# Kernel tuning notes

Hardware: AMD Instinct MI355X
Metric: run time of the kernel (lower is better)

## Reference

```python
import jax, jax.numpy as jnp
import numpy as np

V = 20000
D = 128
N_PAIRS = 65536
LOG_EPS = 1e-8


def setup_inputs() -> dict:
    key = jax.random.key(0)
    k_emb, k_i, k_j = jax.random.split(key, 3)
    # original: tf.random.uniform([V, D], 0.1, -0.1) -> uniform in (-0.1, 0.1)
    embedding = jax.random.uniform(k_emb, (V, D), dtype=jnp.float32) * 0.2 - 0.1
    i_vec = jax.random.randint(k_i, (N_PAIRS,), 0, V, dtype=jnp.int64)
    j_vec = jax.random.randint(k_j, (N_PAIRS,), 0, V, dtype=jnp.int64)
    return {"embedding": embedding, "i_vec": i_vec, "j_vec": j_vec}


def reference(embedding, i_vec, j_vec):
    # norms[i] = exp( sum_j e_i . e_j )  -- full V x V Gram matrix row-reduced
    gram = jnp.matmul(embedding, embedding.T)        # [V, V]
    norms = jnp.exp(jnp.sum(gram, axis=1))           # [V]
    # denoms[p] = exp( e_{i_p} . e_{j_p} )
    denoms = jnp.exp(jnp.sum(embedding[i_vec] * embedding[j_vec], axis=1))  # [N]
    emb_cost = -jnp.log(denoms / norms[i_vec] + LOG_EPS)
    return jnp.mean(emb_cost)
```

## Files before the change

kernel.cpp:

```cpp
#include <hip/hip_runtime.h>
#include <math.h>

#define DIM     128
#define V_ROWS  20000
#define NPAIRS  65536
#define NFLOAT4 (V_ROWS * DIM / 4)

constexpr int K1_BLOCKS  = 256;
constexpr int K1_THREADS = 256;
constexpr int K1_STRIDE  = K1_BLOCKS * K1_THREADS;
constexpr int K3_BLOCKS  = 1024;
constexpr int K3_THREADS = 256;


__global__ __launch_bounds__(K1_THREADS) void k1_colsum(
        const float4* __restrict__ emb4,
        float* __restrict__ partial) {
    const int tid = blockIdx.x * K1_THREADS + threadIdx.x;
    float4 a = make_float4(0.f, 0.f, 0.f, 0.f);
    #pragma unroll
    for (int k = 0; k < 9; ++k) {
        const float4 v = emb4[tid + k * K1_STRIDE];
        a.x += v.x; a.y += v.y; a.z += v.z; a.w += v.w;
    }
    if (tid + 9 * K1_STRIDE < NFLOAT4) {
        const float4 v = emb4[tid + 9 * K1_STRIDE];
        a.x += v.x; a.y += v.y; a.z += v.z; a.w += v.w;
    }
    a.x += __shfl_xor(a.x, 32);
    a.y += __shfl_xor(a.y, 32);
    a.z += __shfl_xor(a.z, 32);
    a.w += __shfl_xor(a.w, 32);

    __shared__ float sm[4][DIM];
    const int wid  = threadIdx.x >> 6;
    const int lane = threadIdx.x & 63;
    const int col  = (threadIdx.x * 4) & 127;
    if (lane < 32) {
        sm[wid][col + 0] = a.x;
        sm[wid][col + 1] = a.y;
        sm[wid][col + 2] = a.z;
        sm[wid][col + 3] = a.w;
    }
    __syncthreads();
    if (threadIdx.x < DIM) {
        partial[blockIdx.x * DIM + threadIdx.x] =
            sm[0][threadIdx.x] + sm[1][threadIdx.x] +
            sm[2][threadIdx.x] + sm[3][threadIdx.x];
    }
}

__global__ __launch_bounds__(1024) void k2_fold(
        const float* __restrict__ partial,
        float* __restrict__ S) {
    const int t   = threadIdx.x;
    const int col = t & 127;
    const int g   = t >> 7;
    float s = 0.f;
    #pragma unroll
    for (int k = 0; k < 32; ++k) {
        s += partial[(g + k * 8) * DIM + col];
    }
    __shared__ float sm[8][DIM];
    sm[g][col] = s;
    __syncthreads();
    if (t < DIM) {
        float tot = 0.f;
        #pragma unroll
        for (int g2 = 0; g2 < 8; ++g2) tot += sm[g2][t];
        S[t] = tot;
    }
}

__global__ __launch_bounds__(K3_THREADS) void k3_pairs(
        const float4* __restrict__ emb4,
        const int* __restrict__ iv,
        const int* __restrict__ jv,
        const float* __restrict__ S,
        float* __restrict__ blockpart) {
    const int lane = threadIdx.x & 63;
    const int wid  = threadIdx.x >> 6;
    const int c    = lane & 15;
    const int grp  = lane >> 4;
    const int gw   = blockIdx.x * 4 + wid;
    const int base = gw * 16;

    const float4* S4 = reinterpret_cast<const float4*>(S);
    const float4 s0 = S4[c * 2], s1 = S4[c * 2 + 1];

    int idxval = 0;
    if (lane < 16)      idxval = iv[base + lane];
    else if (lane < 32) idxval = jv[base + lane - 16];

    float4 A0[4], A1[4], B0[4], B1[4];
    #pragma unroll
    for (int it = 0; it < 4; ++it) {
        const int q = it * 4 + grp;
        const int i = __shfl(idxval, q);
        const int j = __shfl(idxval, 16 + q);
        const float4* ei = emb4 + (size_t)i * 32;
        const float4* ej = emb4 + (size_t)j * 32;
        A0[it] = ei[c * 2]; A1[it] = ei[c * 2 + 1];
        B0[it] = ej[c * 2]; B1[it] = ej[c * 2 + 1];
    }

    float acc = 0.f;
    #pragma unroll
    for (int it = 0; it < 4; ++it) {
        float d = A0[it].x * B0[it].x + A0[it].y * B0[it].y
                + A0[it].z * B0[it].z + A0[it].w * B0[it].w
                + A1[it].x * B1[it].x + A1[it].y * B1[it].y
                + A1[it].z * B1[it].z + A1[it].w * B1[it].w;
        float n = A0[it].x * s0.x + A0[it].y * s0.y
                + A0[it].z * s0.z + A0[it].w * s0.w
                + A1[it].x * s1.x + A1[it].y * s1.y
                + A1[it].z * s1.z + A1[it].w * s1.w;
        #pragma unroll
        for (int off = 8; off > 0; off >>= 1) {
            d += __shfl_xor(d, off);
            n += __shfl_xor(n, off);
        }
        const float cost = -logf(expf(d - n) + 1e-8f);
        if (c == 0) acc += cost;
    }

    acc += __shfl_xor(acc, 16);
    acc += __shfl_xor(acc, 32);

    __shared__ float ls[4];
    if (lane == 0) ls[wid] = acc;
    __syncthreads();
    if (threadIdx.x == 0)
        blockpart[blockIdx.x] = ls[0] + ls[1] + ls[2] + ls[3];
}

__global__ __launch_bounds__(1024) void k4_final(
        const float* __restrict__ blockpart,
        float* __restrict__ out) {
    const int t = threadIdx.x;
    float s = blockpart[t];
    #pragma unroll
    for (int off = 32; off > 0; off >>= 1) s += __shfl_xor(s, off);
    __shared__ float ls[16];
    if ((t & 63) == 0) ls[t >> 6] = s;
    __syncthreads();
    if (t == 0) {
        float tot = 0.f;
        #pragma unroll
        for (int w = 0; w < 16; ++w) tot += ls[w];
        out[0] = tot / (float)NPAIRS;
    }
}

extern "C" void kernel_launch(void* const* d_in, const int* in_sizes, int n_in,
                              void* d_out, int out_size, void* d_ws, size_t ws_size,
                              hipStream_t stream) {
    const float* emb = (const float*)d_in[0];
    const int*   iv  = (const int*)d_in[1];
    const int*   jv  = (const int*)d_in[2];
    float* out = (float*)d_out;

    float* partial   = (float*)d_ws;
    float* S         = partial + K1_BLOCKS * DIM;
    float* blockpart = S + DIM;

    hipLaunchKernelGGL(k1_colsum, dim3(K1_BLOCKS), dim3(K1_THREADS), 0, stream,
                       (const float4*)emb, partial);
    hipLaunchKernelGGL(k2_fold, dim3(1), dim3(1024), 0, stream,
                       partial, S);
    hipLaunchKernelGGL(k3_pairs, dim3(K3_BLOCKS), dim3(K3_THREADS), 0, stream,
                       (const float4*)emb, iv, jv, S, blockpart);
    hipLaunchKernelGGL(k4_final, dim3(1), dim3(1024), 0, stream,
                       blockpart, out);
}
```

Measured before the change: 23.48 us.

## Fuse four kernels into one cooperative kernel with grid-wide syncs

Replaces the colsum, fold, pair-loss and final-reduce launches with a single cooperative kernel of 256 blocks that uses grid.sync between phases. Each block redundantly folds the column partials into shared memory instead of a dedicated single-block kernel, and each wave now processes 64 pairs across four outer iterations. The aim is to remove launch gaps and tiny serial kernels, at the cost of grid-barrier overhead and fewer waves in flight for the gather phase.

```diff
diff --git a/kernel.cpp b/kernel.cpp
--- a/kernel.cpp
+++ b/kernel.cpp
@@ -1,175 +1,164 @@
 #include <hip/hip_runtime.h>
+#include <hip/hip_cooperative_groups.h>
 #include <math.h>
+
+namespace cg = cooperative_groups;
 
 #define DIM     128
 #define V_ROWS  20000
 #define NPAIRS  65536
 #define NFLOAT4 (V_ROWS * DIM / 4)
 
-constexpr int K1_BLOCKS  = 256;
-constexpr int K1_THREADS = 256;
-constexpr int K1_STRIDE  = K1_BLOCKS * K1_THREADS;
-constexpr int K3_BLOCKS  = 1024;
-constexpr int K3_THREADS = 256;
+constexpr int BLOCKS  = 256;
+constexpr int THREADS = 256;
+constexpr int NTHREADS = BLOCKS * THREADS;
+constexpr int TAIL = NFLOAT4 - 9 * NTHREADS;
 
 
-__global__ __launch_bounds__(K1_THREADS) void k1_colsum(
-        const float4* __restrict__ emb4,
-        float* __restrict__ partial) {
-    const int tid = blockIdx.x * K1_THREADS + threadIdx.x;
-    float4 a = make_float4(0.f, 0.f, 0.f, 0.f);
-    #pragma unroll
-    for (int k = 0; k < 9; ++k) {
-        const float4 v = emb4[tid + k * K1_STRIDE];
-        a.x += v.x; a.y += v.y; a.z += v.z; a.w += v.w;
-    }
-    if (tid + 9 * K1_STRIDE < NFLOAT4) {
-        const float4 v = emb4[tid + 9 * K1_STRIDE];
-        a.x += v.x; a.y += v.y; a.z += v.z; a.w += v.w;
-    }
-    a.x += __shfl_xor(a.x, 32);
-    a.y += __shfl_xor(a.y, 32);
-    a.z += __shfl_xor(a.z, 32);
-    a.w += __shfl_xor(a.w, 32);
-
-    __shared__ float sm[4][DIM];
-    const int wid  = threadIdx.x >> 6;
-    const int lane = threadIdx.x & 63;
-    const int col  = (threadIdx.x * 4) & 127;
-    if (lane < 32) {
-        sm[wid][col + 0] = a.x;
-        sm[wid][col + 1] = a.y;
-        sm[wid][col + 2] = a.z;
-        sm[wid][col + 3] = a.w;
-    }
-    __syncthreads();
-    if (threadIdx.x < DIM) {
-        partial[blockIdx.x * DIM + threadIdx.x] =
-            sm[0][threadIdx.x] + sm[1][threadIdx.x] +
-            sm[2][threadIdx.x] + sm[3][threadIdx.x];
-    }
-}
-
-__global__ __launch_bounds__(1024) void k2_fold(
-        const float* __restrict__ partial,
-        float* __restrict__ S) {
-    const int t   = threadIdx.x;
-    const int col = t & 127;
-    const int g   = t >> 7;
-    float s = 0.f;
-    #pragma unroll
-    for (int k = 0; k < 32; ++k) {
-        s += partial[(g + k * 8) * DIM + col];
-    }
-    __shared__ float sm[8][DIM];
-    sm[g][col] = s;
-    __syncthreads();
-    if (t < DIM) {
-        float tot = 0.f;
-        #pragma unroll
-        for (int g2 = 0; g2 < 8; ++g2) tot += sm[g2][t];
-        S[t] = tot;
-    }
-}
-
-__global__ __launch_bounds__(K3_THREADS) void k3_pairs(
+__global__ __launch_bounds__(THREADS) void fused(
         const float4* __restrict__ emb4,
         const int* __restrict__ iv,
         const int* __restrict__ jv,
-        const float* __restrict__ S,
-        float* __restrict__ blockpart) {
+        float* __restrict__ partial,
+        float* __restrict__ blockpart,
+        float* __restrict__ out) {
+    const cg::grid_group grid = cg::this_grid();
     const int lane = threadIdx.x & 63;
     const int wid  = threadIdx.x >> 6;
-    const int c    = lane & 15;
-    const int grp  = lane >> 4;
-    const int gw   = blockIdx.x * 4 + wid;
-    const int base = gw * 16;
 
-    const float4* S4 = reinterpret_cast<const float4*>(S);
-    const float4 s0 = S4[c * 2], s1 = S4[c * 2 + 1];
+    __shared__ float sm[4][DIM];
+    __shared__ float S_lds[DIM];
+    __shared__ float ls[4];
 
-    int idxval = 0;
-    if (lane < 16)      idxval = iv[base + lane];
-    else if (lane < 32) idxval = jv[base + lane - 16];
+    {
+        const int tid = blockIdx.x * THREADS + threadIdx.x;
+        float4 a = make_float4(0.f, 0.f, 0.f, 0.f);
+        #pragma unroll
+        for (int k = 0; k < 9; ++k) {
+            const float4 v = emb4[tid + k * NTHREADS];
+            a.x += v.x; a.y += v.y; a.z += v.z; a.w += v.w;
+        }
+        if (tid < TAIL) {
+            const float4 v = emb4[tid + 9 * NTHREADS];
+            a.x += v.x; a.y += v.y; a.z += v.z; a.w += v.w;
+        }
+        a.x += __shfl_xor(a.x, 32);
+        a.y += __shfl_xor(a.y, 32);
+        a.z += __shfl_xor(a.z, 32);
+        a.w += __shfl_xor(a.w, 32);
 
-    float4 A0[4], A1[4], B0[4], B1[4];
-    #pragma unroll
-    for (int it = 0; it < 4; ++it) {
-        const int q = it * 4 + grp;
-        const int i = __shfl(idxval, q);
-        const int j = __shfl(idxval, 16 + q);
-        const float4* ei = emb4 + (size_t)i * 32;
-        const float4* ej = emb4 + (size_t)j * 32;
-        A0[it] = ei[c * 2]; A1[it] = ei[c * 2 + 1];
-        B0[it] = ej[c * 2]; B1[it] = ej[c * 2 + 1];
+        const int col = (threadIdx.x * 4) & 127;
+        if (lane < 32) {
+            sm[wid][col + 0] = a.x;
+            sm[wid][col + 1] = a.y;
+            sm[wid][col + 2] = a.z;
+            sm[wid][col + 3] = a.w;
+        }
+        __syncthreads();
+        if (threadIdx.x < DIM) {
+            partial[blockIdx.x * DIM + threadIdx.x] =
+                sm[0][threadIdx.x] + sm[1][threadIdx.x] +
+                sm[2][threadIdx.x] + sm[3][threadIdx.x];
+        }
     }
 
-    float acc = 0.f;
-    #pragma unroll
-    for (int it = 0; it < 4; ++it) {
-        float d = A0[it].x * B0[it].x + A0[it].y * B0[it].y
-                + A0[it].z * B0[it].z + A0[it].w * B0[it].w
-                + A1[it].x * B1[it].x + A1[it].y * B1[it].y
-                + A1[it].z * B1[it].z + A1[it].w * B1[it].w;
-        float n = A0[it].x * s0.x + A0[it].y * s0.y
-                + A0[it].z * s0.z + A0[it].w * s0.w
-                + A1[it].x * s1.x + A1[it].y * s1.y
-                + A1[it].z * s1.z + A1[it].w * s1.w;
-        #pragma unroll
-        for (int off = 8; off > 0; off >>= 1) {
-            d += __shfl_xor(d, off);
-            n += __shfl_xor(n, off);
+    grid.sync();
+
+    {
+        const int col = threadIdx.x & 127;
+        const int g   = threadIdx.x >> 7;
+        float s = 0.f;
+        #pragma unroll 8
+        for (int k = 0; k < BLOCKS / 2; ++k) {
+            s += partial[(g + 2 * k) * DIM + col];
         }
-        const float cost = -logf(expf(d - n) + 1e-8f);
-        if (c == 0) acc += cost;
+        __syncthreads();
+        sm[g][col] = s;
+        __syncthreads();
+        if (threadIdx.x < DIM) S_lds[threadIdx.x] = sm[0][threadIdx.x] + sm[1][threadIdx.x];
+        __syncthreads();
     }
 
-    acc += __shfl_xor(acc, 16);
-    acc += __shfl_xor(acc, 32);
+    {
+        const int c   = lane & 15;
+        const int grp = lane >> 4;
+        const int gw  = blockIdx.x * 4 + wid;
+        const int base = gw * 64;
 
-    __shared__ float ls[4];
-    if (lane == 0) ls[wid] = acc;
-    __syncthreads();
-    if (threadIdx.x == 0)
-        blockpart[blockIdx.x] = ls[0] + ls[1] + ls[2] + ls[3];
-}
+        const float4* S4 = reinterpret_cast<const float4*>(S_lds);
+        const float4 s0 = S4[c * 2], s1 = S4[c * 2 + 1];
 
-__global__ __launch_bounds__(1024) void k4_final(
-        const float* __restrict__ blockpart,
-        float* __restrict__ out) {
-    const int t = threadIdx.x;
-    float s = blockpart[t];
-    #pragma unroll
-    for (int off = 32; off > 0; off >>= 1) s += __shfl_xor(s, off);
-    __shared__ float ls[16];
-    if ((t & 63) == 0) ls[t >> 6] = s;
-    __syncthreads();
-    if (t == 0) {
-        float tot = 0.f;
+        const int i64 = iv[base + lane];
+        const int j64 = jv[base + lane];
+
+        float acc = 0.f;
+        for (int ot = 0; ot < 4; ++ot) {
+            float4 A0[4], A1[4], B0[4], B1[4];
+            #pragma unroll
+            for (int it = 0; it < 4; ++it) {
+                const int q = ot * 16 + it * 4 + grp;
+                const int i = __shfl(i64, q);
+                const int j = __shfl(j64, q);
+                const float4* ei = emb4 + (size_t)i * 32;
+                const float4* ej = emb4 + (size_t)j * 32;
+                A0[it] = ei[c * 2]; A1[it] = ei[c * 2 + 1];
+                B0[it] = ej[c * 2]; B1[it] = ej[c * 2 + 1];
+            }
+            #pragma unroll
+            for (int it = 0; it < 4; ++it) {
+                float d = A0[it].x * B0[it].x + A0[it].y * B0[it].y
+                        + A0[it].z * B0[it].z + A0[it].w * B0[it].w
+                        + A1[it].x * B1[it].x + A1[it].y * B1[it].y
+                        + A1[it].z * B1[it].z + A1[it].w * B1[it].w;
+                float n = A0[it].x * s0.x + A0[it].y * s0.y
+                        + A0[it].z * s0.z + A0[it].w * s0.w
+                        + A1[it].x * s1.x + A1[it].y * s1.y
+                        + A1[it].z * s1.z + A1[it].w * s1.w;
+                #pragma unroll
+                for (int off = 8; off > 0; off >>= 1) {
+                    d += __shfl_xor(d, off);
+                    n += __shfl_xor(n, off);
+                }
+                const float cost = -logf(expf(d - n) + 1e-8f);
+                if (c == 0) acc += cost;
+            }
+        }
+        acc += __shfl_xor(acc, 16);
+        acc += __shfl_xor(acc, 32);
+
+        __syncthreads();
+        if (lane == 0) ls[wid] = acc;
+        __syncthreads();
+        if (threadIdx.x == 0)
+            blockpart[blockIdx.x] = ls[0] + ls[1] + ls[2] + ls[3];
+    }
+
+    grid.sync();
+
+    if (blockIdx.x == 0) {
+        float s = blockpart[threadIdx.x];
         #pragma unroll
-        for (int w = 0; w < 16; ++w) tot += ls[w];
-        out[0] = tot / (float)NPAIRS;
+        for (int off = 32; off > 0; off >>= 1) s += __shfl_xor(s, off);
+        if (lane == 0) ls[wid] = s;
+        __syncthreads();
+        if (threadIdx.x == 0)
+            out[0] = (ls[0] + ls[1] + ls[2] + ls[3]) / (float)NPAIRS;
     }
 }
 
 extern "C" void kernel_launch(void* const* d_in, const int* in_sizes, int n_in,
                               void* d_out, int out_size, void* d_ws, size_t ws_size,
                               hipStream_t stream) {
-    const float* emb = (const float*)d_in[0];
-    const int*   iv  = (const int*)d_in[1];
-    const int*   jv  = (const int*)d_in[2];
+    const float4* emb4 = (const float4*)d_in[0];
+    const int*    iv   = (const int*)d_in[1];
+    const int*    jv   = (const int*)d_in[2];
     float* out = (float*)d_out;
 
     float* partial   = (float*)d_ws;
-    float* S         = partial + K1_BLOCKS * DIM;
-    float* blockpart = S + DIM;
+    float* blockpart = partial + BLOCKS * DIM;
 
-    hipLaunchKernelGGL(k1_colsum, dim3(K1_BLOCKS), dim3(K1_THREADS), 0, stream,
-                       (const float4*)emb, partial);
-    hipLaunchKernelGGL(k2_fold, dim3(1), dim3(1024), 0, stream,
-                       partial, S);
-    hipLaunchKernelGGL(k3_pairs, dim3(K3_BLOCKS), dim3(K3_THREADS), 0, stream,
-                       (const float4*)emb, iv, jv, S, blockpart);
-    hipLaunchKernelGGL(k4_final, dim3(1), dim3(1024), 0, stream,
-                       blockpart, out);
+    void* args[] = { (void*)&emb4, (void*)&iv, (void*)&jv,
+                     (void*)&partial, (void*)&blockpart, (void*)&out };
+    hipLaunchCooperativeKernel((const void*)fused, dim3(BLOCKS), dim3(THREADS),
+                               args, 0, stream);
 }
```

Result: slower. 77.92 us (+231.9%).

## Fuse column-sum fold into pairs kernel and double pairs per warp

Applied to the files above, without the earlier changes.

Removes the single-block fold kernel by having every block of the pairs kernel redundantly reduce the 256 partial column sums into shared memory. Each warp now processes 32 pairs in two batches, halving the grid to 512 blocks, and the final reduction shrinks to 256 threads. This saves one kernel launch and its serial dependency, but each block re-reads the 128 KB of partials, which adds L2 traffic and startup latency per block.

```diff
diff --git a/kernel.cpp b/kernel.cpp
--- a/kernel.cpp
+++ b/kernel.cpp
@@ -9,8 +9,10 @@
 constexpr int K1_BLOCKS  = 256;
 constexpr int K1_THREADS = 256;
 constexpr int K1_STRIDE  = K1_BLOCKS * K1_THREADS;
-constexpr int K3_BLOCKS  = 1024;
-constexpr int K3_THREADS = 256;
+constexpr int K1_TAIL    = NFLOAT4 - 9 * K1_STRIDE;
+
+constexpr int K2_BLOCKS  = 512;
+constexpr int K2_THREADS = 256;
 
 
 __global__ __launch_bounds__(K1_THREADS) void k1_colsum(
@@ -23,7 +25,7 @@
         const float4 v = emb4[tid + k * K1_STRIDE];
         a.x += v.x; a.y += v.y; a.z += v.z; a.w += v.w;
     }
-    if (tid + 9 * K1_STRIDE < NFLOAT4) {
+    if (tid < K1_TAIL) {
         const float4 v = emb4[tid + 9 * K1_STRIDE];
         a.x += v.x; a.y += v.y; a.z += v.z; a.w += v.w;
     }
@@ -50,126 +52,118 @@
     }
 }
 
-__global__ __launch_bounds__(1024) void k2_fold(
-        const float* __restrict__ partial,
-        float* __restrict__ S) {
-    const int t   = threadIdx.x;
-    const int col = t & 127;
-    const int g   = t >> 7;
-    float s = 0.f;
-    #pragma unroll
-    for (int k = 0; k < 32; ++k) {
-        s += partial[(g + k * 8) * DIM + col];
-    }
-    __shared__ float sm[8][DIM];
-    sm[g][col] = s;
-    __syncthreads();
-    if (t < DIM) {
-        float tot = 0.f;
-        #pragma unroll
-        for (int g2 = 0; g2 < 8; ++g2) tot += sm[g2][t];
-        S[t] = tot;
-    }
-}
-
-__global__ __launch_bounds__(K3_THREADS) void k3_pairs(
+__global__ __launch_bounds__(K2_THREADS) void k2_pairs(
         const float4* __restrict__ emb4,
         const int* __restrict__ iv,
         const int* __restrict__ jv,
-        const float* __restrict__ S,
+        const float* __restrict__ partial,
         float* __restrict__ blockpart) {
     const int lane = threadIdx.x & 63;
     const int wid  = threadIdx.x >> 6;
+
+    __shared__ float sm[2][DIM];
+    __shared__ float S_lds[DIM];
+    __shared__ float ls[4];
+
+    {
+        const int col = threadIdx.x & 127;
+        const int g   = threadIdx.x >> 7;
+        float s0 = 0.f, s1 = 0.f, s2 = 0.f, s3 = 0.f;
+        #pragma unroll 8
+        for (int k = 0; k < 32; ++k) {
+            s0 += partial[(g + 8 * k + 0) * DIM + col];
+            s1 += partial[(g + 8 * k + 2) * DIM + col];
+            s2 += partial[(g + 8 * k + 4) * DIM + col];
+            s3 += partial[(g + 8 * k + 6) * DIM + col];
+        }
+        sm[g][col] = (s0 + s1) + (s2 + s3);
+        __syncthreads();
+        if (threadIdx.x < DIM)
+            S_lds[threadIdx.x] = sm[0][threadIdx.x] + sm[1][threadIdx.x];
+        __syncthreads();
+    }
+
     const int c    = lane & 15;
     const int grp  = lane >> 4;
     const int gw   = blockIdx.x * 4 + wid;
-    const int base = gw * 16;
+    const int base = gw * 32;
 
-    const float4* S4 = reinterpret_cast<const float4*>(S);
+    const float4* S4 = reinterpret_cast<const float4*>(S_lds);
     const float4 s0 = S4[c * 2], s1 = S4[c * 2 + 1];
 
-    int idxval = 0;
-    if (lane < 16)      idxval = iv[base + lane];
-    else if (lane < 32) idxval = jv[base + lane - 16];
-
-    float4 A0[4], A1[4], B0[4], B1[4];
-    #pragma unroll
-    for (int it = 0; it < 4; ++it) {
-        const int q = it * 4 + grp;
-        const int i = __shfl(idxval, q);
-        const int j = __shfl(idxval, 16 + q);
-        const float4* ei = emb4 + (size_t)i * 32;
-        const float4* ej = emb4 + (size_t)j * 32;
-        A0[it] = ei[c * 2]; A1[it] = ei[c * 2 + 1];
-        B0[it] = ej[c * 2]; B1[it] = ej[c * 2 + 1];
-    }
+    const int idxval = (lane < 32) ? iv[base + lane] : jv[base + lane - 32];
 
     float acc = 0.f;
     #pragma unroll
-    for (int it = 0; it < 4; ++it) {
-        float d = A0[it].x * B0[it].x + A0[it].y * B0[it].y
-                + A0[it].z * B0[it].z + A0[it].w * B0[it].w
-                + A1[it].x * B1[it].x + A1[it].y * B1[it].y
-                + A1[it].z * B1[it].z + A1[it].w * B1[it].w;
-        float n = A0[it].x * s0.x + A0[it].y * s0.y
-                + A0[it].z * s0.z + A0[it].w * s0.w
-                + A1[it].x * s1.x + A1[it].y * s1.y
-                + A1[it].z * s1.z + A1[it].w * s1.w;
+    for (int ot = 0; ot < 2; ++ot) {
+        float4 A0[4], A1[4], B0[4], B1[4];
         #pragma unroll
-        for (int off = 8; off > 0; off >>= 1) {
-            d += __shfl_xor(d, off);
-            n += __shfl_xor(n, off);
+        for (int it = 0; it < 4; ++it) {
+            const int q = ot * 16 + it * 4 + grp;
+            const int i = __shfl(idxval, q);
+            const int j = __shfl(idxval, 32 + q);
+            const float4* ei = emb4 + (size_t)i * 32;
+            const float4* ej = emb4 + (size_t)j * 32;
+            A0[it] = ei[c * 2]; A1[it] = ei[c * 2 + 1];
+            B0[it] = ej[c * 2]; B1[it] = ej[c * 2 + 1];
         }
-        const float cost = -logf(expf(d - n) + 1e-8f);
-        if (c == 0) acc += cost;
+        #pragma unroll
+        for (int it = 0; it < 4; ++it) {
+            float d = A0[it].x * B0[it].x + A0[it].y * B0[it].y
+                    + A0[it].z * B0[it].z + A0[it].w * B0[it].w
+                    + A1[it].x * B1[it].x + A1[it].y * B1[it].y
+                    + A1[it].z * B1[it].z + A1[it].w * B1[it].w;
+            float n = A0[it].x * s0.x + A0[it].y * s0.y
+                    + A0[it].z * s0.z + A0[it].w * s0.w
+                    + A1[it].x * s1.x + A1[it].y * s1.y
+                    + A1[it].z * s1.z + A1[it].w * s1.w;
+            #pragma unroll
+            for (int off = 8; off > 0; off >>= 1) {
+                d += __shfl_xor(d, off);
+                n += __shfl_xor(n, off);
+            }
+            const float cost = -logf(expf(d - n) + 1e-8f);
+            if (c == 0) acc += cost;
+        }
     }
-
     acc += __shfl_xor(acc, 16);
     acc += __shfl_xor(acc, 32);
 
-    __shared__ float ls[4];
     if (lane == 0) ls[wid] = acc;
     __syncthreads();
     if (threadIdx.x == 0)
         blockpart[blockIdx.x] = ls[0] + ls[1] + ls[2] + ls[3];
 }
 
-__global__ __launch_bounds__(1024) void k4_final(
+__global__ __launch_bounds__(256) void k3_final(
         const float* __restrict__ blockpart,
         float* __restrict__ out) {
     const int t = threadIdx.x;
-    float s = blockpart[t];
+    float s = blockpart[t] + blockpart[t + 256];
     #pragma unroll
     for (int off = 32; off > 0; off >>= 1) s += __shfl_xor(s, off);
-    __shared__ float ls[16];
+    __shared__ float ls[4];
     if ((t & 63) == 0) ls[t >> 6] = s;
     __syncthreads();
-    if (t == 0) {
-        float tot = 0.f;
-        #pragma unroll
-        for (int w = 0; w < 16; ++w) tot += ls[w];
-        out[0] = tot / (float)NPAIRS;
-    }
+    if (t == 0)
+        out[0] = (ls[0] + ls[1] + ls[2] + ls[3]) / (float)NPAIRS;
 }
 
 extern "C" void kernel_launch(void* const* d_in, const int* in_sizes, int n_in,
                               void* d_out, int out_size, void* d_ws, size_t ws_size,
                               hipStream_t stream) {
-    const float* emb = (const float*)d_in[0];
-    const int*   iv  = (const int*)d_in[1];
-    const int*   jv  = (const int*)d_in[2];
+    const float4* emb4 = (const float4*)d_in[0];
+    const int*    iv   = (const int*)d_in[1];
+    const int*    jv   = (const int*)d_in[2];
     float* out = (float*)d_out;
 
     float* partial   = (float*)d_ws;
-    float* S         = partial + K1_BLOCKS * DIM;
-    float* blockpart = S + DIM;
+    float* blockpart = partial + K1_BLOCKS * DIM;
 
     hipLaunchKernelGGL(k1_colsum, dim3(K1_BLOCKS), dim3(K1_THREADS), 0, stream,
-                       (const float4*)emb, partial);
-    hipLaunchKernelGGL(k2_fold, dim3(1), dim3(1024), 0, stream,
-                       partial, S);
-    hipLaunchKernelGGL(k3_pairs, dim3(K3_BLOCKS), dim3(K3_THREADS), 0, stream,
-                       (const float4*)emb, iv, jv, S, blockpart);
-    hipLaunchKernelGGL(k4_final, dim3(1), dim3(1024), 0, stream,
+                       emb4, partial);
+    hipLaunchKernelGGL(k2_pairs, dim3(K2_BLOCKS), dim3(K2_THREADS), 0, stream,
+                       emb4, iv, jv, partial, blockpart);
+    hipLaunchKernelGGL(k3_final, dim3(1), dim3(256), 0, stream,
                        blockpart, out);
 }
```

After: 21.98 us. 1.07x faster.
